# Optimization experiments

Hardware: AMD Instinct MI355X
Metric: run time of the kernel (lower is better)

Reference implementation:

```python
import jax, jax.numpy as jnp
import numpy as np

H = 8  # heads, hard-coded in the original module


def setup_inputs() -> dict:
    key = jax.random.key(0)
    ks = jax.random.split(key, 7)
    B, Lq, Lkv = 4, 2048, 512
    dim_q, dim_kv = 1024, 768
    q = jax.random.normal(ks[0], (B, Lq, dim_q), dtype=jnp.float32)
    kv = jax.random.normal(ks[1], (B, Lkv, dim_kv), dtype=jnp.float32)
    # Linear weights stored as [in, out] so y = x @ W (math-equivalent to torch Linear)
    Wq = jax.random.normal(ks[2], (dim_q, dim_q), dtype=jnp.float32) / np.sqrt(dim_q)
    Wk = jax.random.normal(ks[3], (dim_kv, dim_q), dtype=jnp.float32) / np.sqrt(dim_kv)
    Wv = jax.random.normal(ks[4], (dim_kv, dim_q), dtype=jnp.float32) / np.sqrt(dim_kv)
    Wo = jax.random.normal(ks[5], (dim_q, dim_q), dtype=jnp.float32) / np.sqrt(dim_q)
    bo = jax.random.normal(ks[6], (dim_q,), dtype=jnp.float32) * 0.01
    return {"q": q, "kv": kv, "Wq": Wq, "Wk": Wk, "Wv": Wv, "Wo": Wo, "bo": bo}


def reference(q, kv, Wq, Wk, Wv, Wo, bo):
    B, Lq, dim_q = q.shape
    hd = dim_q // H
    scale = jnp.asarray(hd, q.dtype) ** -0.5
    # projections
    qp = q @ Wq   # [B, Lq, dim_q]
    kp = kv @ Wk  # [B, Lkv, dim_q]
    vp = kv @ Wv  # [B, Lkv, dim_q]
    # split heads: [B, L, H, hd]
    qh = qp.reshape(B, Lq, H, hd)
    kh = kp.reshape(B, kv.shape[1], H, hd)
    vh = vp.reshape(B, kv.shape[1], H, hd)
    # scaled attention scores and softmax
    scores = jnp.einsum("bqhd,bkhd->bhqk", qh, kh) * scale
    attn = jax.nn.softmax(scores, axis=-1)
    out = jnp.einsum("bhqk,bkhd->bqhd", attn, vh).reshape(B, Lq, dim_q)
    return out @ Wo + bo
```

## Files before the change

### kernel.cpp

```cpp
#include <hip/hip_runtime.h>


typedef unsigned short u16;
typedef unsigned int u32;
using short8  = __attribute__((ext_vector_type(8))) short;
using floatx4 = __attribute__((ext_vector_type(4))) float;

__device__ inline u16 f2bf(float x) {
  union { float f; u32 u; } v; v.f = x;
  u32 r = (v.u + 0x7fffu + ((v.u >> 16) & 1u)) >> 16;
  return (u16)r;
}

__device__ inline float fast_exp2(float x) {
#if __has_builtin(__builtin_amdgcn_exp2f)
  return __builtin_amdgcn_exp2f(x);
#else
  return exp2f(x);
#endif
}

#define MFMA(a, b, c) __builtin_amdgcn_mfma_f32_16x16x32_bf16(a, b, c, 0, 0, 0)

__device__ inline void async_lds16(const void* g, void* l) {
  __builtin_amdgcn_global_load_lds(
      (const __attribute__((address_space(1))) void*)g,
      (__attribute__((address_space(3))) void*)l, 16, 0, 0);
}

#define WAIT_VM(n) { asm volatile("s_waitcnt vmcnt(" #n ")" ::: "memory"); \
                     __builtin_amdgcn_sched_barrier(0); }
#define WAIT_LGKM0 { asm volatile("s_waitcnt lgkmcnt(0)" ::: "memory"); \
                     __builtin_amdgcn_sched_barrier(0); }
#define SBAR       { __builtin_amdgcn_s_barrier(); \
                     __builtin_amdgcn_sched_barrier(0); }

__device__ __forceinline__
void transpose_body(int bid, const float* __restrict__ Wq, const float* __restrict__ Wk,
                    const float* __restrict__ Wv, const float* __restrict__ Wo,
                    u16* __restrict__ WqT, u16* __restrict__ WkvT, u16* __restrict__ WoT,
                    float* __restrict__ tile ) {
  const int z = bid >> 8;
  const float* W; u16* Wt; int K;
  if      (z == 0) { W = Wq; Wt = WqT;               K = 1024; }
  else if (z == 1) { W = Wk; Wt = WkvT;              K = 768;  }
  else if (z == 2) { W = Wv; Wt = WkvT + 1024 * 768; K = 768;  }
  else             { W = Wo; Wt = WoT;               K = 1024; }
  const int k0 = ((bid >> 4) & 15) * 64, n0 = (bid & 15) * 64;
  if (k0 >= K) return;
  const int N = 1024;
  const int t = threadIdx.x;
  for (int p = 0; p < 4; ++p) {
    int cid = p * 256 + t;
    int row = cid >> 4, c = cid & 15;
    float4 v = *(const float4*)&W[(long)(k0 + row) * N + n0 + c * 4];
    tile[row * 68 + c * 4 + 0] = v.x; tile[row * 68 + c * 4 + 1] = v.y;
    tile[row * 68 + c * 4 + 2] = v.z; tile[row * 68 + c * 4 + 3] = v.w;
  }
  __syncthreads();
  for (int p = 0; p < 2; ++p) {
    int oc = p * 256 + t;
    int n = oc >> 3, c = oc & 7;
    u16 tmp[8];
    for (int s = 0; s < 8; ++s) tmp[s] = f2bf(tile[(c * 8 + s) * 68 + n]);
    *(short8*)&Wt[(long)(n0 + n) * K + k0 + c * 8] = *(short8*)tmp;
  }
}

__global__ __launch_bounds__(256)
void k_prep(const float* __restrict__ q, const float* __restrict__ kv,
            u16* __restrict__ q_bf, u16* __restrict__ kv_bf,
            const float* __restrict__ Wq, const float* __restrict__ Wk,
            const float* __restrict__ Wv, const float* __restrict__ Wo,
            u16* __restrict__ WqT, u16* __restrict__ WkvT, u16* __restrict__ WoT) {
  __shared__ __align__(16) float tile[64 * 68];
  const int bid = blockIdx.x;
  if (bid < 4864) {
    int i = bid * 256 + threadIdx.x;
    const float* src; u16* dst; int idx;
    if (i < 1048576) { src = q;  dst = q_bf;  idx = i; }
    else             { src = kv; dst = kv_bf; idx = i - 1048576; }
    float4 a = ((const float4*)src)[2 * idx];
    float4 b = ((const float4*)src)[2 * idx + 1];
    u16 t[8] = {f2bf(a.x), f2bf(a.y), f2bf(a.z), f2bf(a.w),
                f2bf(b.x), f2bf(b.y), f2bf(b.z), f2bf(b.w)};
    ((short8*)dst)[idx] = *(short8*)t;
  } else {
    transpose_body(bid - 4864, Wq, Wk, Wv, Wo, WqT, WkvT, WoT, tile);
  }
}

__device__ __forceinline__
void gemm_body(const u16* __restrict__ A, const u16* __restrict__ Bt,
               u16* __restrict__ Cb, float* __restrict__ Cf,
               const float* __restrict__ bias, u16* __restrict__ vt_out,
               int K, int ldc, int lin, int mt_per_xcd, u16* smem) {
  const int tid  = threadIdx.x;
  const int wave = tid >> 6, lane = tid & 63;
  const int l15  = lane & 15, quad = lane >> 4;
  const int wm   = (wave >> 1) * 64, wn = (wave & 1) * 64;
  const int xcd  = lin & 7, slot = lin >> 3;
  const int mt   = xcd * mt_per_xcd + (slot % mt_per_xcd);
  const int nti  = slot / mt_per_xcd;
  const long m0  = (long)mt * 128, n0 = (long)nti * 128;

  const int pl  = lane >> 3;
  const int gg  = (lane & 7) ^ pl;
  const int ro  = pl * 2 + (gg >> 2);
  const int co  = (gg & 3) * 8;
  const u16* Aw = A  + (m0 + wave * 32 + ro) * (long)K + co;
  const u16* Bw = Bt + (n0 + wave * 32 + ro) * (long)K + co;
  const int rdo  = ((((l15 & 1) << 2) | quad) ^ (l15 >> 1)) * 8;
  const int aoff = wm * 32 + (l15 >> 1) * 64 + rdo;
  const int boff = wn * 32 + (l15 >> 1) * 64 + rdo;

#define STAGE_G(Bse, kk)                                                   \
  { u16* Ab_ = (Bse); u16* Bb_ = (Bse) + 4096;                             \
    async_lds16(Aw + (kk),                Ab_ + wave * 1024);              \
    async_lds16(Aw + 16 * (long)K + (kk), Ab_ + wave * 1024 + 512);        \
    async_lds16(Bw + (kk),                Bb_ + wave * 1024);              \
    async_lds16(Bw + 16 * (long)K + (kk), Bb_ + wave * 1024 + 512); }

  floatx4 acc[4][4] = {};
  const int NS = K >> 5;
  STAGE_G(smem, 0);
  STAGE_G(smem + 8192, 32);
  int cb = 0, nb = 2;
  for (int s = 0; s < NS; ++s) {
    u16* Ac = smem + cb * 8192; u16* Bc = Ac + 4096;
    if (s + 2 < NS) {
      STAGE_G(smem + nb * 8192, (s + 2) * 32);
      WAIT_VM(8);
    } else if (s + 1 < NS) {
      WAIT_VM(4);
    } else {
      WAIT_VM(0);
    }
    SBAR;
    short8 af[4], bfr[4];
    for (int i = 0; i < 4; ++i) af[i]  = *(const short8*)&Ac[aoff + i * 512];
    for (int j = 0; j < 4; ++j) bfr[j] = *(const short8*)&Bc[boff + j * 512];
    for (int i = 0; i < 4; ++i)
      for (int j = 0; j < 4; ++j)
        acc[i][j] = MFMA(af[i], bfr[j], acc[i][j]);
    WAIT_LGKM0;
    SBAR;
    cb = (cb == 2) ? 0 : cb + 1;
    nb = (nb == 2) ? 0 : nb + 1;
  }
#undef STAGE_G

  if (Cf) {
    for (int i = 0; i < 4; ++i)
      for (int j = 0; j < 4; ++j) {
        long row = m0 + wm + i * 16 + quad * 4;
        long col = n0 + wn + j * 16 + l15;
        float b = bias ? bias[col] : 0.f;
        for (int r = 0; r < 4; ++r) Cf[(row + r) * (long)ldc + col] = acc[i][j][r] + b;
      }
    return;
  }
  for (int i = 0; i < 4; ++i)
    for (int j = 0; j < 4; ++j)
      for (int r = 0; r < 4; ++r)
        smem[(wm + i * 16 + quad * 4 + r) * 138 + wn + j * 16 + l15] = f2bf(acc[i][j][r]);
  __syncthreads();
  if (vt_out && nti >= 8) {
    const int h  = nti - 8;
    const int bq = (int)(m0 >> 9);
    const int l0 = (int)(m0 & 511);
    u16* vbase = vt_out + ((long)(bq * 8 + h) * 128) * 512;
    for (int p = 0; p < 8; ++p) {
      int cid = p * 256 + tid;
      int d = cid >> 4, c = cid & 15;
      u16 tmp[8];
      for (int s = 0; s < 8; ++s) tmp[s] = smem[(c * 8 + s) * 138 + d];
      *(short8*)&vbase[(long)d * 512 + l0 + c * 8] = *(short8*)tmp;
    }
  } else {
    for (int p = 0; p < 8; ++p) {
      int cid = p * 256 + tid;
      int row = cid >> 4, c = cid & 15;
      short8 v = *(const short8*)&smem[row * 138 + c * 8];
      *(short8*)&Cb[(m0 + row) * (long)ldc + n0 + c * 8] = v;
    }
  }
}

__global__ __launch_bounds__(256)
void k_proj_qkv(const u16* __restrict__ q_bf, const u16* __restrict__ WqT,
                const u16* __restrict__ kv_bf, const u16* __restrict__ WkvT,
                u16* __restrict__ qp, u16* __restrict__ kp, u16* __restrict__ vT) {
  __shared__ __align__(16) u16 smem[24576];
  const int bid = blockIdx.x;
  if (bid < 512)
    gemm_body(q_bf, WqT, qp, nullptr, nullptr, nullptr, 1024, 1024, bid, 8, smem);
  else
    gemm_body(kv_bf, WkvT, kp, nullptr, nullptr, vT, 768, 1024, bid - 512, 2, smem);
}

__global__ __launch_bounds__(512)
void k_attn(const u16* __restrict__ qp, const u16* __restrict__ kp,
            const u16* __restrict__ vT, u16* __restrict__ ctx) {
  __shared__ __align__(16) u16 smem[24576];
  u16* Ks = smem;
  u16* Vs = smem + 8192;
  const int lin  = blockIdx.x;
  const int tid  = threadIdx.x;
  const int wave = tid >> 6, lane = tid & 63;
  u16* Pw = smem + 16384 + wave * 1024;
  const int l15  = lane & 15, quad = lane >> 4;
  const int xcd  = lin & 7, slot = lin >> 3;
  const int pairIdx = xcd * 4 + (slot & 3);
  const int b = pairIdx >> 3, h = pairIdx & 7;
  const int qtile = slot >> 2;
  const long rowbase = (long)b * 2048 + qtile * 128 + wave * 16;
  const float sc = 0.08838834764831845f * 1.4426950408889634f;

  short8 aQ[4];
  for (int dc = 0; dc < 4; ++dc)
    aQ[dc] = *(const short8*)&qp[(rowbase + l15) * 1024 + h * 128 + dc * 32 + quad * 8];

  floatx4 O[8] = {};
  float lsum[4] = {};
  const u16* kpb   = kp + ((long)b * 512) * 1024 + h * 128;
  const u16* vbase = vT + ((long)(b * 8 + h) * 128) * 512;

  const int krow = lane >> 4;
  const int kpos = lane & 15;
  const int vrow = lane >> 3;
  const int vpos = lane & 7;

#define STAGE_K(t)                                                             \
  for (int i = 0; i < 2; ++i) {                                                \
    int inst = wave * 2 + i;                                                   \
    int row  = inst * 4 + krow;                                                \
    int g    = kpos ^ (row & 15);                                              \
    async_lds16(kpb + (long)((t) * 64 + row) * 1024 + g * 8, &Ks[inst * 512]); \
  }
#define STAGE_V(t)                                                             \
  for (int i = 0; i < 2; ++i) {                                                \
    int inst = wave * 2 + i;                                                   \
    int d    = inst * 8 + vrow;                                                \
    int g    = vpos ^ (d & 7);                                                 \
    async_lds16(vbase + (long)d * 512 + (t) * 64 + g * 8, &Vs[inst * 512]);    \
  }

  STAGE_K(0);
  STAGE_V(0);
  for (int t = 0; t < 8; ++t) {
    WAIT_VM(2);
    SBAR;
    floatx4 S[4] = {};
    __builtin_amdgcn_s_setprio(1);
    for (int dc = 0; dc < 4; ++dc)
      for (int ks = 0; ks < 4; ++ks) {
        int k = ks * 16 + l15;
        short8 bk = *(const short8*)&Ks[k * 128 + (((dc * 4 + quad) ^ l15) * 8)];
        S[ks] = MFMA(aQ[dc], bk, S[ks]);
      }
    __builtin_amdgcn_s_setprio(0);
    WAIT_LGKM0;
    SBAR;
    if (t < 7) STAGE_K(t + 1);
    for (int ks = 0; ks < 4; ++ks)
      for (int r = 0; r < 4; ++r) {
        float p = fast_exp2(S[ks][r] * sc);
        lsum[r] += p;
        int row = quad * 4 + r;
        int g   = (ks * 2 + (l15 >> 3)) ^ (row & 7);
        Pw[row * 64 + g * 8 + (l15 & 7)] = f2bf(p);
      }
    short8 aP[2];
    for (int kc = 0; kc < 2; ++kc)
      aP[kc] = *(const short8*)&Pw[l15 * 64 + (((kc * 4 + quad) ^ (l15 & 7)) * 8)];
    if (t < 7) { WAIT_VM(2); }
    else       { WAIT_VM(0); }
    SBAR;
    __builtin_amdgcn_s_setprio(1);
    for (int j = 0; j < 8; ++j) {
      int d = j * 16 + l15;
      short8 bV0 = *(const short8*)&Vs[d * 64 + ((quad ^ (l15 & 7)) * 8)];
      short8 bV1 = *(const short8*)&Vs[d * 64 + (((4 + quad) ^ (l15 & 7)) * 8)];
      O[j] = MFMA(aP[0], bV0, O[j]);
      O[j] = MFMA(aP[1], bV1, O[j]);
    }
    __builtin_amdgcn_s_setprio(0);
    WAIT_LGKM0;
    SBAR;
    if (t < 7) STAGE_V(t + 1);
  }
#undef STAGE_K
#undef STAGE_V

  for (int r = 0; r < 4; ++r) {
    float sum = lsum[r];
    for (int off = 1; off < 16; off <<= 1) sum += __shfl_xor(sum, off);
    lsum[r] = 1.f / sum;
  }
  for (int j = 0; j < 8; ++j)
    for (int r = 0; r < 4; ++r)
      ctx[(rowbase + quad * 4 + r) * 1024 + h * 128 + j * 16 + l15] =
          f2bf(O[j][r] * lsum[r]);
}

__global__ __launch_bounds__(256)
void k_oproj(const u16* __restrict__ ctx, const u16* __restrict__ WoT,
             float* __restrict__ out, const float* __restrict__ bo) {
  __shared__ __align__(16) u16 smem[24576];
  gemm_body(ctx, WoT, nullptr, out, bo, nullptr, 1024, 1024, blockIdx.x, 8, smem);
}

extern "C" void kernel_launch(void* const* d_in, const int* in_sizes, int n_in,
                              void* d_out, int out_size, void* d_ws, size_t ws_size,
                              hipStream_t stream) {
  const float* q  = (const float*)d_in[0];
  const float* kv = (const float*)d_in[1];
  const float* Wq = (const float*)d_in[2];
  const float* Wk = (const float*)d_in[3];
  const float* Wv = (const float*)d_in[4];
  const float* Wo = (const float*)d_in[5];
  const float* bo = (const float*)d_in[6];
  float* out = (float*)d_out;

  char* ws = (char*)d_ws;
  u16* q_bf  = (u16*)(ws + 0);
  u16* kv_bf = (u16*)(ws + 16777216);
  u16* WqT   = (u16*)(ws + 19922944);
  u16* WkvT  = (u16*)(ws + 22020096);
  u16* WoT   = (u16*)(ws + 25165824);
  u16* qp    = (u16*)(ws + 27262976);
  u16* kp    = (u16*)(ws + 44040192);
  u16* vT    = (u16*)(ws + 52428800);
  u16* ctx   = (u16*)(ws + 56623104);

  k_prep<<<5888, 256, 0, stream>>>(q, kv, q_bf, kv_bf, Wq, Wk, Wv, Wo,
                                   WqT, WkvT, WoT);
  k_proj_qkv<<<768, 256, 0, stream>>>(q_bf, WqT, kv_bf, WkvT, qp, kp, vT);
  k_attn<<<512, 512, 0, stream>>>(qp, kp, vT, ctx);
  k_oproj<<<512, 256, 0, stream>>>(ctx, WoT, out, bo);
}
```

Measured before the change: 181.7 us.

## Fuse fp32-to-bf16 activation conversion into QKV projection GEMM loads

Removes the separate pass that converted q and kv to bf16 in workspace. The QKV projection GEMM now loads fp32 activations into registers, converts them with packed bf16 conversion instructions and writes them into double-buffered LDS, while weights still stream asynchronously into LDS. The Wo transpose moves into extra blocks of the projection kernel and the weight-transpose kernel shrinks to Wq/Wk/Wv only. This avoids a full round trip of the activations through memory, at the cost of register-staged A loads, a two-stage pipeline and twice the fp32 read bytes inside the GEMM.

```diff
diff --git a/kernel.cpp b/kernel.cpp
--- a/kernel.cpp
+++ b/kernel.cpp
@@ -10,6 +10,12 @@
   union { float f; u32 u; } v; v.f = x;
   u32 r = (v.u + 0x7fffu + ((v.u >> 16) & 1u)) >> 16;
   return (u16)r;
+}
+
+__device__ inline u32 cvtpk(float a, float b) {
+  u32 r;
+  asm("v_cvt_pk_bf16_f32 %0, %1, %2" : "=v"(r) : "v"(a), "v"(b));
+  return r;
 }
 
 __device__ inline float fast_exp2(float x) {
@@ -68,32 +74,131 @@
 }
 
 __global__ __launch_bounds__(256)
-void k_prep(const float* __restrict__ q, const float* __restrict__ kv,
-            u16* __restrict__ q_bf, u16* __restrict__ kv_bf,
-            const float* __restrict__ Wq, const float* __restrict__ Wk,
-            const float* __restrict__ Wv, const float* __restrict__ Wo,
-            u16* __restrict__ WqT, u16* __restrict__ WkvT, u16* __restrict__ WoT) {
+void k_wt(const float* __restrict__ Wq, const float* __restrict__ Wk,
+          const float* __restrict__ Wv,
+          u16* __restrict__ WqT, u16* __restrict__ WkvT) {
   __shared__ __align__(16) float tile[64 * 68];
-  const int bid = blockIdx.x;
-  if (bid < 4864) {
-    int i = bid * 256 + threadIdx.x;
-    const float* src; u16* dst; int idx;
-    if (i < 1048576) { src = q;  dst = q_bf;  idx = i; }
-    else             { src = kv; dst = kv_bf; idx = i - 1048576; }
-    float4 a = ((const float4*)src)[2 * idx];
-    float4 b = ((const float4*)src)[2 * idx + 1];
-    u16 t[8] = {f2bf(a.x), f2bf(a.y), f2bf(a.z), f2bf(a.w),
-                f2bf(b.x), f2bf(b.y), f2bf(b.z), f2bf(b.w)};
-    ((short8*)dst)[idx] = *(short8*)t;
+  transpose_body(blockIdx.x, Wq, Wk, Wv, nullptr, WqT, WkvT, nullptr, tile);
+}
+
+__device__ __forceinline__
+void gemm_f32a_body(const float* __restrict__ Af, const u16* __restrict__ Bt,
+                    u16* __restrict__ Cb, u16* __restrict__ vt_out,
+                    int K, int ldc, int lin, int mt_per_xcd, u16* smem) {
+  const int tid  = threadIdx.x;
+  const int wave = tid >> 6, lane = tid & 63;
+  const int l15  = lane & 15, quad = lane >> 4;
+  const int wm   = (wave >> 1) * 64, wn = (wave & 1) * 64;
+  const int xcd  = lin & 7, slot = lin >> 3;
+  const int mt   = xcd * mt_per_xcd + (slot % mt_per_xcd);
+  const int nti  = slot / mt_per_xcd;
+  const long m0  = (long)mt * 128, n0 = (long)nti * 128;
+
+  const int pl  = lane >> 3;
+  const int gg  = (lane & 7) ^ pl;
+  const int ro  = pl * 2 + (gg >> 2);
+  const int co  = (gg & 3) * 8;
+  const u16* Bw = Bt + (n0 + wave * 32 + ro) * (long)K + co;
+
+  const int rl  = lane >> 1;
+  const int kh  = lane & 1;
+  const float* Awf = Af + (m0 + wave * 32 + rl) * (long)K + kh * 16;
+  const int p    = wave * 16 + (rl >> 1);
+  const int g0   = (rl & 1) * 4 + kh * 2;
+  const int off0 = p * 64 + ((g0 ^ (p & 7)) * 8);
+  const int off1 = p * 64 + (((g0 + 1) ^ (p & 7)) * 8);
+
+  const int rdo  = ((((l15 & 1) << 2) | quad) ^ (l15 >> 1)) * 8;
+  const int aoff = wm * 32 + (l15 >> 1) * 64 + rdo;
+  const int boff = wn * 32 + (l15 >> 1) * 64 + rdo;
+
+  u16* const buf0 = smem;
+  u16* const buf1 = smem + 8192;
+
+#define LOADA(a0, a1, a2, a3, kk) {                                            \
+    const float4* s_ = (const float4*)(Awf + (kk));                            \
+    a0 = s_[0]; a1 = s_[1]; a2 = s_[2]; a3 = s_[3]; }
+#define STAGEB(bb, kk) {                                                       \
+    async_lds16(Bw + (kk),                (bb) + 4096 + wave * 1024);          \
+    async_lds16(Bw + 16 * (long)K + (kk), (bb) + 4096 + wave * 1024 + 512); }
+#define WRITEA(bb, a0, a1, a2, a3) { u32 w_[8];                                \
+    w_[0] = cvtpk(a0.x, a0.y); w_[1] = cvtpk(a0.z, a0.w);                      \
+    w_[2] = cvtpk(a1.x, a1.y); w_[3] = cvtpk(a1.z, a1.w);                      \
+    w_[4] = cvtpk(a2.x, a2.y); w_[5] = cvtpk(a2.z, a2.w);                      \
+    w_[6] = cvtpk(a3.x, a3.y); w_[7] = cvtpk(a3.z, a3.w);                      \
+    *(short8*)&(bb)[off0] = *(short8*)&w_[0];                                  \
+    *(short8*)&(bb)[off1] = *(short8*)&w_[4]; }
+#define COMPUTE(bb) { short8 af[4], bfr[4];                                    \
+    for (int i = 0; i < 4; ++i) af[i]  = *(const short8*)&(bb)[aoff + i * 512];\
+    for (int j = 0; j < 4; ++j)                                                \
+      bfr[j] = *(const short8*)&(bb)[4096 + boff + j * 512];                   \
+    for (int i = 0; i < 4; ++i)                                                \
+      for (int j = 0; j < 4; ++j)                                              \
+        acc[i][j] = MFMA(af[i], bfr[j], acc[i][j]); }
+
+  floatx4 acc[4][4] = {};
+  float4 rA0, rA1, rA2, rA3, rB0, rB1, rB2, rB3;
+  const int NS = K >> 5;
+
+  LOADA(rA0, rA1, rA2, rA3, 0);
+  STAGEB(buf0, 0);
+  LOADA(rB0, rB1, rB2, rB3, 32);
+  WAIT_VM(6);
+  WRITEA(buf0, rA0, rA1, rA2, rA3);
+  WAIT_LGKM0;
+
+#define ITER(s, bc, bn, c0, c1, c2, c3, n0_, n1_, n2_, n3_) {                  \
+    if ((s) + 1 < NS) STAGEB(bn, ((s) + 1) * 32);                              \
+    if ((s) + 2 < NS) LOADA(n0_, n1_, n2_, n3_, ((s) + 2) * 32);               \
+    if ((s) + 2 < NS)      { WAIT_VM(6); }                                     \
+    else if ((s) + 1 < NS) { WAIT_VM(2); }                                     \
+    else                   { WAIT_VM(0); }                                     \
+    SBAR;                                                                      \
+    if ((s) + 1 < NS) WRITEA(bn, c0, c1, c2, c3);                              \
+    COMPUTE(bc);                                                               \
+    WAIT_LGKM0;                                                                \
+    SBAR; }
+
+  for (int sp = 0; sp < NS; sp += 2) {
+    ITER(sp,     buf0, buf1, rB0, rB1, rB2, rB3, rA0, rA1, rA2, rA3);
+    ITER(sp + 1, buf1, buf0, rA0, rA1, rA2, rA3, rB0, rB1, rB2, rB3);
+  }
+#undef ITER
+#undef LOADA
+#undef STAGEB
+#undef WRITEA
+#undef COMPUTE
+
+  for (int i = 0; i < 4; ++i)
+    for (int j = 0; j < 4; ++j)
+      for (int r = 0; r < 4; ++r)
+        smem[(wm + i * 16 + quad * 4 + r) * 138 + wn + j * 16 + l15] = f2bf(acc[i][j][r]);
+  __syncthreads();
+  if (vt_out && nti >= 8) {
+    const int h  = nti - 8;
+    const int bq = (int)(m0 >> 9);
+    const int l0 = (int)(m0 & 511);
+    u16* vbase = vt_out + ((long)(bq * 8 + h) * 128) * 512;
+    for (int pp = 0; pp < 8; ++pp) {
+      int cid = pp * 256 + tid;
+      int d = cid >> 4, c = cid & 15;
+      u16 tmp[8];
+      for (int s = 0; s < 8; ++s) tmp[s] = smem[(c * 8 + s) * 138 + d];
+      *(short8*)&vbase[(long)d * 512 + l0 + c * 8] = *(short8*)tmp;
+    }
   } else {
-    transpose_body(bid - 4864, Wq, Wk, Wv, Wo, WqT, WkvT, WoT, tile);
+    for (int pp = 0; pp < 8; ++pp) {
+      int cid = pp * 256 + tid;
+      int row = cid >> 4, c = cid & 15;
+      short8 v = *(const short8*)&smem[row * 138 + c * 8];
+      *(short8*)&Cb[(m0 + row) * (long)ldc + n0 + c * 8] = v;
+    }
   }
 }
 
 __device__ __forceinline__
 void gemm_body(const u16* __restrict__ A, const u16* __restrict__ Bt,
-               u16* __restrict__ Cb, float* __restrict__ Cf,
-               const float* __restrict__ bias, u16* __restrict__ vt_out,
+               float* __restrict__ Cf, const float* __restrict__ bias,
                int K, int ldc, int lin, int mt_per_xcd, u16* smem) {
   const int tid  = threadIdx.x;
   const int wave = tid >> 6, lane = tid & 63;
@@ -150,53 +255,29 @@
   }
 #undef STAGE_G
 
-  if (Cf) {
-    for (int i = 0; i < 4; ++i)
-      for (int j = 0; j < 4; ++j) {
-        long row = m0 + wm + i * 16 + quad * 4;
-        long col = n0 + wn + j * 16 + l15;
-        float b = bias ? bias[col] : 0.f;
-        for (int r = 0; r < 4; ++r) Cf[(row + r) * (long)ldc + col] = acc[i][j][r] + b;
-      }
-    return;
-  }
   for (int i = 0; i < 4; ++i)
-    for (int j = 0; j < 4; ++j)
-      for (int r = 0; r < 4; ++r)
-        smem[(wm + i * 16 + quad * 4 + r) * 138 + wn + j * 16 + l15] = f2bf(acc[i][j][r]);
-  __syncthreads();
-  if (vt_out && nti >= 8) {
-    const int h  = nti - 8;
-    const int bq = (int)(m0 >> 9);
-    const int l0 = (int)(m0 & 511);
-    u16* vbase = vt_out + ((long)(bq * 8 + h) * 128) * 512;
-    for (int p = 0; p < 8; ++p) {
-      int cid = p * 256 + tid;
-      int d = cid >> 4, c = cid & 15;
-      u16 tmp[8];
-      for (int s = 0; s < 8; ++s) tmp[s] = smem[(c * 8 + s) * 138 + d];
-      *(short8*)&vbase[(long)d * 512 + l0 + c * 8] = *(short8*)tmp;
+    for (int j = 0; j < 4; ++j) {
+      long row = m0 + wm + i * 16 + quad * 4;
+      long col = n0 + wn + j * 16 + l15;
+      float b = bias ? bias[col] : 0.f;
+      for (int r = 0; r < 4; ++r) Cf[(row + r) * (long)ldc + col] = acc[i][j][r] + b;
     }
-  } else {
-    for (int p = 0; p < 8; ++p) {
-      int cid = p * 256 + tid;
-      int row = cid >> 4, c = cid & 15;
-      short8 v = *(const short8*)&smem[row * 138 + c * 8];
-      *(short8*)&Cb[(m0 + row) * (long)ldc + n0 + c * 8] = v;
-    }
-  }
 }
 
 __global__ __launch_bounds__(256)
-void k_proj_qkv(const u16* __restrict__ q_bf, const u16* __restrict__ WqT,
-                const u16* __restrict__ kv_bf, const u16* __restrict__ WkvT,
+void k_proj_qkv(const float* __restrict__ q, const float* __restrict__ kv,
+                const u16* __restrict__ WqT, const u16* __restrict__ WkvT,
+                const float* __restrict__ Wo, u16* __restrict__ WoT,
                 u16* __restrict__ qp, u16* __restrict__ kp, u16* __restrict__ vT) {
-  __shared__ __align__(16) u16 smem[24576];
+  __shared__ __align__(16) u16 smem[17664];
   const int bid = blockIdx.x;
   if (bid < 512)
-    gemm_body(q_bf, WqT, qp, nullptr, nullptr, nullptr, 1024, 1024, bid, 8, smem);
+    gemm_f32a_body(q, WqT, qp, nullptr, 1024, 1024, bid, 8, smem);
+  else if (bid < 768)
+    gemm_f32a_body(kv, WkvT, kp, vT, 768, 1024, bid - 512, 2, smem);
   else
-    gemm_body(kv_bf, WkvT, kp, nullptr, nullptr, vT, 768, 1024, bid - 512, 2, smem);
+    transpose_body(bid, nullptr, nullptr, nullptr, Wo,
+                   nullptr, nullptr, WoT, (float*)smem);
 }
 
 __global__ __launch_bounds__(512)
@@ -308,7 +389,7 @@
 void k_oproj(const u16* __restrict__ ctx, const u16* __restrict__ WoT,
              float* __restrict__ out, const float* __restrict__ bo) {
   __shared__ __align__(16) u16 smem[24576];
-  gemm_body(ctx, WoT, nullptr, out, bo, nullptr, 1024, 1024, blockIdx.x, 8, smem);
+  gemm_body(ctx, WoT, out, bo, 1024, 1024, blockIdx.x, 8, smem);
 }
 
 extern "C" void kernel_launch(void* const* d_in, const int* in_sizes, int n_in,
@@ -324,8 +405,6 @@
   float* out = (float*)d_out;
 
   char* ws = (char*)d_ws;
-  u16* q_bf  = (u16*)(ws + 0);
-  u16* kv_bf = (u16*)(ws + 16777216);
   u16* WqT   = (u16*)(ws + 19922944);
   u16* WkvT  = (u16*)(ws + 22020096);
   u16* WoT   = (u16*)(ws + 25165824);
@@ -334,9 +413,8 @@
   u16* vT    = (u16*)(ws + 52428800);
   u16* ctx   = (u16*)(ws + 56623104);
 
-  k_prep<<<5888, 256, 0, stream>>>(q, kv, q_bf, kv_bf, Wq, Wk, Wv, Wo,
-                                   WqT, WkvT, WoT);
-  k_proj_qkv<<<768, 256, 0, stream>>>(q_bf, WqT, kv_bf, WkvT, qp, kp, vT);
+  k_wt<<<768, 256, 0, stream>>>(Wq, Wk, Wv, WqT, WkvT);
+  k_proj_qkv<<<1024, 256, 0, stream>>>(q, kv, WqT, WkvT, Wo, WoT, qp, kp, vT);
   k_attn<<<512, 512, 0, stream>>>(qp, kp, vT, ctx);
   k_oproj<<<512, 256, 0, stream>>>(ctx, WoT, out, bo);
 }
```

After: 193.7 us. +6.6%, slower.
